# Optimization experiments

Hardware: AMD Instinct MI355X
Metric: run time of the kernel (lower is better)

The kernel has to match this reference:

```python
import jax, jax.numpy as jnp
import numpy as np

# BQQ block dims: Y_sign (p,j,k,m,l), Z_sign (p,j,k,l,n); in=k*n=4096, out=j*m=4096
P, J, K, M, L, N = 2, 32, 32, 128, 16, 128
ACT_BITS = 8  # activation quantization bits


def setup_inputs() -> dict:
    key = jax.random.key(0)
    ks = jax.random.split(key, 7)
    x = jax.random.normal(ks[0], (1, 512, K * N), dtype=jnp.float32)
    # sign matrices in {-1,+1}
    Y_sign = jnp.where(jax.random.normal(ks[1], (P, J, K, M, L)) >= 0, 1.0, -1.0).astype(jnp.float32)
    Z_sign = jnp.where(jax.random.normal(ks[2], (P, J, K, L, N)) >= 0, 1.0, -1.0).astype(jnp.float32)
    # per-block positive scales (abs-mean in the original, so strictly > 0)
    Y_scale = jax.random.uniform(ks[3], (P, J, K, 1, 1), minval=0.01, maxval=0.1, dtype=jnp.float32)
    Z_scale = jax.random.uniform(ks[4], (P, J, K, 1, 1), minval=0.01, maxval=0.1, dtype=jnp.float32)
    A = jax.random.normal(ks[5], (P, J, K, 4), dtype=jnp.float32) * 0.1
    bias = jax.random.normal(ks[6], (J * M,), dtype=jnp.float32) * 0.1
    return {"input": x, "Y_sign": Y_sign, "Z_sign": Z_sign,
            "Y_scale": Y_scale, "Z_scale": Z_scale, "A": A, "bias": bias}


def reference(input, Y_sign, Z_sign, Y_scale, Z_scale, A, bias):
    # --- activation quantization (act_bits = 8, simple round, no STE) ---
    qmax = float(2 ** (ACT_BITS - 1) - 1)  # 127
    x_max = jnp.max(input)
    x_min = jnp.min(input)
    act_scale = jnp.maximum((x_max - x_min) / (2.0 * qmax), 1e-8)
    X = jnp.clip(jnp.round(input / act_scale), -qmax, qmax) * act_scale

    # --- dequantize sign * scale ---
    Y_q = Y_sign * Y_scale  # (p,j,k,m,l)
    Z_q = Z_sign * Z_scale  # (p,j,k,l,n)

    orig_shape = X.shape[:-1]
    X_kn = X.reshape(-1, K, N)  # (B,k,n)

    # chained block einsums
    T = jnp.einsum('bkn,pjkln->bpjkl', X_kn, Z_q)          # (B,p,j,k,l)
    core = jnp.einsum('pjkml,bpjkl->bpjkm', Y_q, T)        # (B,p,j,k,m)

    # quant_bias=True correction terms: A[...,0..3] = (a,b,c,d)
    out1 = jnp.einsum('bpjkm,pjk->bjm', core, A[..., 0])

    Y_sum = Y_q.sum(axis=-1)                               # (p,j,k,m)
    B_coef = jnp.einsum('pjk,pjkm->jkm', A[..., 1], Y_sum)
    Sx = X_kn.sum(axis=-1)                                 # (B,k)
    out2 = jnp.einsum('bk,jkm->bjm', Sx, B_coef)

    Zs = Z_q.sum(axis=-2)                                  # (p,j,k,n)
    Tz = jnp.einsum('bkn,pjkn->bpjk', X_kn, Zs)
    out3 = jnp.einsum('bpjk,pjk->bj', Tz, A[..., 2])

    D_coef = A[..., 3].sum(axis=0)                         # (j,k)
    out4 = jnp.einsum('bk,jk->bj', Sx, D_coef)

    out_bjm = out1 + out2 + (out3 + out4)[:, :, None]      # (B,j,m)
    out_2d = out_bjm.reshape(-1, J * M) + bias
    return out_2d.reshape(*orig_shape, J * M)
```

## Files before the change

### kernel.cpp

```cpp
#include <hip/hip_runtime.h>
#include <hip/hip_bf16.h>

typedef __attribute__((ext_vector_type(4))) float f32x4;
typedef __attribute__((ext_vector_type(8))) short bf16x8;
typedef __attribute__((ext_vector_type(4))) unsigned int u32x4;

#define GLOBAL_AS __attribute__((address_space(1)))
#define LDS_AS __attribute__((address_space(3)))

static __device__ __forceinline__ unsigned short f2bf(float f) {
  __hip_bfloat16 h = __float2bfloat16(f);
  return __builtin_bit_cast(unsigned short, h);
}
static __device__ __forceinline__ float bf2f(unsigned short u) {
  unsigned int v = ((unsigned int)u) << 16;
  return __builtin_bit_cast(float, v);
}
static __device__ __forceinline__ void load_lds16(const void* g, void* l) {
  __builtin_amdgcn_global_load_lds((GLOBAL_AS void*)g, (LDS_AS void*)l, 16, 0, 0);
}

__global__ __launch_bounds__(256) void k_minmax_part(const float* __restrict__ x,
                                                     float* __restrict__ part) {
  int tid = blockIdx.x * 256 + threadIdx.x;
  const float4* xv = (const float4*)x;
  float mn = 3.4e38f, mx = -3.4e38f;
#pragma unroll
  for (int rep = 0; rep < 8; ++rep) {
    float4 v = xv[tid + rep * 65536];
    mn = fminf(mn, fminf(fminf(v.x, v.y), fminf(v.z, v.w)));
    mx = fmaxf(mx, fmaxf(fmaxf(v.x, v.y), fmaxf(v.z, v.w)));
  }
#pragma unroll
  for (int o = 32; o > 0; o >>= 1) {
    mn = fminf(mn, __shfl_down(mn, o));
    mx = fmaxf(mx, __shfl_down(mx, o));
  }
  __shared__ float smn[4], smx[4];
  int lane = threadIdx.x & 63, w = threadIdx.x >> 6;
  if (lane == 0) { smn[w] = mn; smx[w] = mx; }
  __syncthreads();
  if (threadIdx.x == 0) {
    mn = fminf(fminf(smn[0], smn[1]), fminf(smn[2], smn[3]));
    mx = fmaxf(fmaxf(smx[0], smx[1]), fmaxf(smx[2], smx[3]));
    part[2 * blockIdx.x] = mn;
    part[2 * blockIdx.x + 1] = mx;
  }
}

__global__ __launch_bounds__(256) void k_fused(const float* __restrict__ x,
                                               const float* __restrict__ part,
                                               const float* __restrict__ Ysg,
                                               const float* __restrict__ Zsg,
                                               const float* __restrict__ Ysc,
                                               const float* __restrict__ Zsc,
                                               const float* __restrict__ Acoef,
                                               float* __restrict__ scl,
                                               unsigned short* __restrict__ xq,
                                               unsigned short* __restrict__ W) {
  const int t = threadIdx.x;
  if (blockIdx.x < 1024) {
    const int jk = blockIdx.x;
    __shared__ unsigned short Yb[2 * 128 * 24];
    __shared__ unsigned short Zb[128 * 36];
    __shared__ float B1p[2][128];
    __shared__ float C1[128];
    float cf0[2], cf2[2], cf4[2];
    float Dv;
    {
      float ys0 = Ysc[jk], zs0 = Zsc[jk], ys1 = Ysc[1024 + jk], zs1 = Zsc[1024 + jk];
      const float* A0p = Acoef + (size_t)jk * 4;
      const float* A1p = Acoef + (size_t)(1024 + jk) * 4;
      cf0[0] = A0p[0] * ys0 * zs0; cf0[1] = A1p[0] * ys1 * zs1;
      cf2[0] = A0p[1] * ys0;       cf2[1] = A1p[1] * ys1;
      cf4[0] = A0p[2] * zs0;       cf4[1] = A1p[2] * zs1;
      Dv = A0p[3] + A1p[3];
    }
#pragma unroll
    for (int rep = 0; rep < 4; ++rep) {
      int q = rep * 256 + t;
      int l0 = (q & 3) * 4, m = (q >> 2) & 127, p = q >> 9;
      float4 v = *(const float4*)(Ysg + (size_t)(p * 1024 + jk) * 2048 + m * 16 + l0);
      float s4 = v.x + v.y + v.z + v.w;
      s4 += __shfl_xor(s4, 1);
      s4 += __shfl_xor(s4, 2);
      if ((t & 3) == 0) B1p[p][m] = s4;
      float c0 = cf0[p];
      ushort4 o = make_ushort4(f2bf(c0 * v.x), f2bf(c0 * v.y), f2bf(c0 * v.z), f2bf(c0 * v.w));
      *(ushort4*)&Yb[(p * 128 + m) * 24 + l0] = o;
    }
#pragma unroll
    for (int rep = 0; rep < 4; ++rep) {
      int q = rep * 256 + t;
      int n0 = (q & 31) * 4, l = (q >> 5) & 15, p = q >> 9;
      float4 v = *(const float4*)(Zsg + (size_t)(p * 1024 + jk) * 2048 + l * 128 + n0);
      int pl = p * 16 + l;
      Zb[(n0 + 0) * 36 + pl] = f2bf(v.x);
      Zb[(n0 + 1) * 36 + pl] = f2bf(v.y);
      Zb[(n0 + 2) * 36 + pl] = f2bf(v.z);
      Zb[(n0 + 3) * 36 + pl] = f2bf(v.w);
    }
    __syncthreads();
    if (t < 128) {
      float s0 = 0.f, s1 = 0.f;
#pragma unroll
      for (int l = 0; l < 16; ++l) {
        s0 += bf2f(Zb[t * 36 + l]);
        s1 += bf2f(Zb[t * 36 + 16 + l]);
      }
      C1[t] = cf4[0] * s0 + cf4[1] * s1;
    }
    __syncthreads();
    const int lane = t & 63, wid = t >> 6;
    const int wm = wid >> 1, wn = wid & 1;
    const int grp = lane >> 4;
    bf16x8 af[4], bfr[4];
#pragma unroll
    for (int fm = 0; fm < 4; ++fm) {
      int m = wm * 64 + fm * 16 + (lane & 15);
      af[fm] = *(const bf16x8*)((const char*)Yb + ((grp >> 1) * 128 + m) * 48 + (grp & 1) * 16);
    }
#pragma unroll
    for (int fn = 0; fn < 4; ++fn) {
      int n = wn * 64 + fn * 16 + (lane & 15);
      const char* zp = (const char*)Zb + n * 72 + grp * 16;
      uint2 z0 = *(const uint2*)zp;
      uint2 z1 = *(const uint2*)(zp + 8);
      u32x4 zw; zw[0] = z0.x; zw[1] = z0.y; zw[2] = z1.x; zw[3] = z1.y;
      bfr[fn] = __builtin_bit_cast(bf16x8, zw);
    }
    f32x4 acc[4][4];
#pragma unroll
    for (int fm = 0; fm < 4; ++fm)
#pragma unroll
      for (int fn = 0; fn < 4; ++fn)
        acc[fm][fn] = __builtin_amdgcn_mfma_f32_16x16x32_bf16(af[fm], bfr[fn], (f32x4)(0.f), 0, 0, 0);
    const int j = jk >> 5, k = jk & 31;
    float c1v[4];
#pragma unroll
    for (int fn = 0; fn < 4; ++fn) c1v[fn] = C1[wn * 64 + fn * 16 + (lane & 15)];
#pragma unroll
    for (int fm = 0; fm < 4; ++fm) {
#pragma unroll
      for (int i = 0; i < 4; ++i) {
        int row = wm * 64 + fm * 16 + (grp)*4 + i;
        float b1v = cf2[0] * B1p[0][row] + cf2[1] * B1p[1][row] + Dv;
        size_t rowoff = (size_t)(j * 128 + row) * 4096 + (size_t)(k * 128);
#pragma unroll
        for (int fn = 0; fn < 4; ++fn) {
          int col = wn * 64 + fn * 16 + (lane & 15);
          W[rowoff + col] = f2bf(acc[fm][fn][i] + b1v + c1v[fn]);
        }
      }
    }
  } else {
    const int qb = blockIdx.x - 1024;
    float2 v2 = ((const float2*)part)[t];
    float mn = v2.x, mx = v2.y;
#pragma unroll
    for (int o = 32; o > 0; o >>= 1) {
      mn = fminf(mn, __shfl_down(mn, o));
      mx = fmaxf(mx, __shfl_down(mx, o));
    }
    __shared__ float smn2[4], smx2[4], ssc[1];
    int lane = t & 63, w = t >> 6;
    if (lane == 0) { smn2[w] = mn; smx2[w] = mx; }
    __syncthreads();
    if (t == 0) {
      mn = fminf(fminf(smn2[0], smn2[1]), fminf(smn2[2], smn2[3]));
      mx = fmaxf(fmaxf(smx2[0], smx2[1]), fmaxf(smx2[2], smx2[3]));
      ssc[0] = fmaxf((mx - mn) / 254.0f, 1e-8f);
      if (qb == 0) scl[0] = ssc[0];
    }
    __syncthreads();
    const float s = ssc[0];
    int i = qb * 256 + t;
    float4 v = ((const float4*)x)[i];
    float a = fminf(fmaxf(rintf(v.x / s), -127.f), 127.f);
    float b = fminf(fmaxf(rintf(v.y / s), -127.f), 127.f);
    float c = fminf(fmaxf(rintf(v.z / s), -127.f), 127.f);
    float d = fminf(fmaxf(rintf(v.w / s), -127.f), 127.f);
    ((ushort4*)xq)[i] = make_ushort4(f2bf(a), f2bf(b), f2bf(c), f2bf(d));
  }
}

__global__ __launch_bounds__(512) void k_gemm(const unsigned short* __restrict__ Xq,
                                              const unsigned short* __restrict__ W,
                                              unsigned short* __restrict__ P) {
  __shared__ unsigned short Al[2][256 * 64];
  __shared__ unsigned short Bl[2][256 * 64];
  const int t = threadIdx.x, lane = t & 63, wid = t >> 6;
  const int wg = (blockIdx.x & 7) * 32 + (blockIdx.x >> 3);
  const int sk = wg >> 5;
  const int bm = (wg >> 4) & 1;
  const int bn = wg & 15;
  const int wm = wid >> 2, wn = wid & 3;
  const int kbase = sk * 512;
  f32x4 acc[8][4];
#pragma unroll
  for (int a = 0; a < 8; ++a)
#pragma unroll
    for (int b = 0; b < 4; ++b) acc[a][b] = (f32x4)(0.f);

  const int lr = lane >> 3;
  const int lcb = (lane & 7) * 16;

  auto STAGE_A2 = [&](int buf, int kt, int half) {
    const int k0 = kbase + kt * 64;
#pragma unroll
    for (int c = 0; c < 2; ++c) {
      int chunk = wid * 4 + half * 2 + c;
      int r = chunk * 8 + lr;
      int colb = lcb ^ ((r & 7) << 4);
      load_lds16(Xq + ((size_t)(bm * 256 + r) << 12) + k0 + (colb >> 1), &Al[buf][chunk * 512]);
    }
  };
  auto STAGE_B2 = [&](int buf, int kt, int half) {
    const int k0 = kbase + kt * 64;
#pragma unroll
    for (int c = 0; c < 2; ++c) {
      int chunk = wid * 4 + half * 2 + c;
      int r = chunk * 8 + lr;
      int colb = lcb ^ ((r & 7) << 4);
      load_lds16(W + ((size_t)(bn * 256 + r) << 12) + k0 + (colb >> 1), &Bl[buf][chunk * 512]);
    }
  };

  STAGE_A2(0, 0, 0); STAGE_A2(0, 0, 1);
  STAGE_B2(0, 0, 0); STAGE_B2(0, 0, 1);

  for (int it = 0; it < 8; ++it) {
    const int cur = it & 1, nxt = cur ^ 1;
    const int ktn = (it + 1) & 7;
#pragma unroll
    for (int sp = 0; sp < 4; ++sp) {
      if (sp == 0)      STAGE_A2(nxt, ktn, 0);
      else if (sp == 1) STAGE_A2(nxt, ktn, 1);
      else if (sp == 2) STAGE_B2(nxt, ktn, 0);
      else              STAGE_B2(nxt, ktn, 1);
      if (sp == 0) {
        __builtin_amdgcn_sched_barrier(0);
        asm volatile("s_waitcnt vmcnt(2)" ::: "memory");
        __builtin_amdgcn_sched_barrier(0);
        __builtin_amdgcn_s_barrier();
        __builtin_amdgcn_sched_barrier(0);
      }
      const int fmh = sp & 1;
      const int ksh = sp >> 1;
      bf16x8 af[4], bfr[4];
#pragma unroll
      for (int f = 0; f < 4; ++f) {
        int fm = fmh * 4 + f;
        int r = wm * 128 + fm * 16 + (lane & 15);
        int colb = (ksh * 64 + ((lane >> 4) * 16)) ^ ((r & 7) << 4);
        af[f] = *(const bf16x8*)((const char*)&Al[cur][0] + r * 128 + colb);
      }
#pragma unroll
      for (int fn = 0; fn < 4; ++fn) {
        int r = wn * 64 + fn * 16 + (lane & 15);
        int colb = (ksh * 64 + ((lane >> 4) * 16)) ^ ((r & 7) << 4);
        bfr[fn] = *(const bf16x8*)((const char*)&Bl[cur][0] + r * 128 + colb);
      }
      __builtin_amdgcn_sched_barrier(0);
      __builtin_amdgcn_s_setprio(1);
#pragma unroll
      for (int f = 0; f < 4; ++f)
#pragma unroll
        for (int fn = 0; fn < 4; ++fn)
          acc[fmh * 4 + f][fn] =
              __builtin_amdgcn_mfma_f32_16x16x32_bf16(af[f], bfr[fn], acc[fmh * 4 + f][fn], 0, 0, 0);
      __builtin_amdgcn_s_setprio(0);
      __builtin_amdgcn_sched_barrier(0);
    }
    __builtin_amdgcn_s_barrier();
  }

  unsigned short* Pk = P + (size_t)sk * 2097152;
  const int blkL = bm * 16 + bn;
#pragma unroll
  for (int fm = 0; fm < 8; ++fm) {
#pragma unroll
    for (int fn = 0; fn < 4; ++fn) {
      int idx = (((blkL * 8 + wid) * 32 + fm * 4 + fn) * 64) + lane;
      ushort4 o = make_ushort4(f2bf(acc[fm][fn][0]), f2bf(acc[fm][fn][1]),
                               f2bf(acc[fm][fn][2]), f2bf(acc[fm][fn][3]));
      ((ushort4*)Pk)[idx] = o;
    }
  }
}

__global__ __launch_bounds__(256) void k_epi(float* __restrict__ out,
                                             const unsigned short* __restrict__ P,
                                             const float* __restrict__ scl,
                                             const float* __restrict__ bias) {
  int g = blockIdx.x * 256 + threadIdx.x;
  const int lane = g & 63;
  const int ff = (g >> 6) & 31;
  const int fn = ff & 3, fm = ff >> 2;
  const int wid = (g >> 11) & 7;
  const int blkL = g >> 14;
  const int bm = blkL >> 4, bn = blkL & 15;
  const int wm = wid >> 2, wn = wid & 3;
  const int row0 = bm * 256 + wm * 128 + fm * 16 + ((lane >> 4) << 2);
  const int col = bn * 256 + wn * 64 + fn * 16 + (lane & 15);
  const float s = scl[0];
  const float bv = bias[col];
  float sum[4] = {0.f, 0.f, 0.f, 0.f};
#pragma unroll
  for (int k = 0; k < 8; ++k) {
    ushort4 p = ((const ushort4*)(P + (size_t)k * 2097152))[g];
    sum[0] += bf2f(p.x); sum[1] += bf2f(p.y); sum[2] += bf2f(p.z); sum[3] += bf2f(p.w);
  }
#pragma unroll
  for (int i = 0; i < 4; ++i) out[(size_t)(row0 + i) * 4096 + col] = sum[i] * s + bv;
}

__global__ __launch_bounds__(512) void k_gemm_fb(const unsigned short* __restrict__ Xq,
                                                 const unsigned short* __restrict__ W,
                                                 const float* __restrict__ scl,
                                                 const float* __restrict__ bias,
                                                 float* __restrict__ out) {
  __shared__ unsigned short Al[4][128 * 64];
  __shared__ unsigned short Bl[4][64 * 64];
  const int t = threadIdx.x, lane = t & 63, wid = t >> 6;
  const int wg = (blockIdx.x & 7) * 32 + (blockIdx.x >> 3);
  const int bm = wg & 3;
  const int bn = wg >> 2;
  const int wm = wid >> 1, wn = wid & 1;
  f32x4 acc[2][2];
#pragma unroll
  for (int a = 0; a < 2; ++a)
#pragma unroll
    for (int b = 0; b < 2; ++b) acc[a][b] = (f32x4)(0.f);
  const int lr = lane >> 3;
  const int lcb = (lane & 7) * 16;
  auto STAGE = [&](int buf, int kt) {
    const int k0 = kt * 64;
#pragma unroll
    for (int c = 0; c < 2; ++c) {
      int chunk = wid * 2 + c;
      int r = chunk * 8 + lr;
      int colb = lcb ^ ((r & 7) << 4);
      load_lds16(Xq + ((size_t)(bm * 128 + r) << 12) + k0 + (colb >> 1), &Al[buf][chunk * 512]);
    }
    {
      int r = wid * 8 + lr;
      int colb = lcb ^ ((r & 7) << 4);
      load_lds16(W + ((size_t)(bn * 64 + r) << 12) + k0 + (colb >> 1), &Bl[buf][wid * 512]);
    }
  };
  auto COMPUTE = [&](int buf) {
#pragma unroll
    for (int ks = 0; ks < 2; ++ks) {
      bf16x8 af[2], bfr[2];
#pragma unroll
      for (int fm = 0; fm < 2; ++fm) {
        int r = wm * 32 + fm * 16 + (lane & 15);
        int colb = (ks * 64 + ((lane >> 4) * 16)) ^ ((r & 7) << 4);
        af[fm] = *(const bf16x8*)((const char*)&Al[buf][0] + r * 128 + colb);
      }
#pragma unroll
      for (int fn = 0; fn < 2; ++fn) {
        int r = wn * 32 + fn * 16 + (lane & 15);
        int colb = (ks * 64 + ((lane >> 4) * 16)) ^ ((r & 7) << 4);
        bfr[fn] = *(const bf16x8*)((const char*)&Bl[buf][0] + r * 128 + colb);
      }
#pragma unroll
      for (int fm = 0; fm < 2; ++fm)
#pragma unroll
        for (int fn = 0; fn < 2; ++fn)
          acc[fm][fn] = __builtin_amdgcn_mfma_f32_16x16x32_bf16(af[fm], bfr[fn], acc[fm][fn], 0, 0, 0);
    }
  };
  STAGE(0, 0); STAGE(1, 1); STAGE(2, 2);
  for (int t64 = 0; t64 < 64; ++t64) {
    STAGE((t64 + 3) & 3, (t64 + 3) & 63);
    __builtin_amdgcn_sched_barrier(0);
    asm volatile("s_waitcnt vmcnt(9)" ::: "memory");
    __builtin_amdgcn_sched_barrier(0);
    __builtin_amdgcn_s_barrier();
    __builtin_amdgcn_sched_barrier(0);
    COMPUTE(t64 & 3);
    __builtin_amdgcn_sched_barrier(0);
    __builtin_amdgcn_s_barrier();
  }
  const float s = scl[0];
#pragma unroll
  for (int fn = 0; fn < 2; ++fn) {
    int col = bn * 64 + wn * 32 + fn * 16 + (lane & 15);
    float bv = bias[col];
#pragma unroll
    for (int fm = 0; fm < 2; ++fm) {
#pragma unroll
      for (int i = 0; i < 4; ++i) {
        int row = bm * 128 + wm * 32 + fm * 16 + (lane >> 4) * 4 + i;
        out[(size_t)row * 4096 + col] = acc[fm][fn][i] * s + bv;
      }
    }
  }
}

extern "C" void kernel_launch(void* const* d_in, const int* in_sizes, int n_in,
                              void* d_out, int out_size, void* d_ws, size_t ws_size,
                              hipStream_t stream) {
  const float* x    = (const float*)d_in[0];
  const float* Ysg  = (const float*)d_in[1];
  const float* Zsg  = (const float*)d_in[2];
  const float* Ysc  = (const float*)d_in[3];
  const float* Zsc  = (const float*)d_in[4];
  const float* A    = (const float*)d_in[5];
  const float* bias = (const float*)d_in[6];
  float* out = (float*)d_out;

  char* ws = (char*)d_ws;
  float* scl  = (float*)ws;
  float* part = (float*)(ws + 256);
  unsigned short* Xq = (unsigned short*)(ws + 65536);
  unsigned short* W  = (unsigned short*)(ws + 65536 + (size_t)4194304);
  unsigned short* P  = (unsigned short*)(ws + 65536 + (size_t)4194304 + (size_t)33554432);

  k_minmax_part<<<dim3(256), dim3(256), 0, stream>>>(x, part);
  k_fused<<<dim3(3072), dim3(256), 0, stream>>>(x, part, Ysg, Zsg, Ysc, Zsc, A, scl, Xq, W);
  if (ws_size >= (size_t)65536 + 4194304 + 33554432 + 33554432) {
    k_gemm<<<dim3(256), dim3(512), 0, stream>>>(Xq, W, P);
    k_epi<<<dim3(2048), dim3(256), 0, stream>>>(out, P, scl, bias);
  } else {
    k_gemm_fb<<<dim3(256), dim3(512), 0, stream>>>(Xq, W, scl, bias, out);
  }
}
```

Before: 57.97 us.

## Restructure GEMM K-loop to reuse B fragments and interleave LDS reads with MFMA

Replaces the unrolled four-subphase loop with an explicit schedule. B fragments are now read once per K-half and reused across both M-halves, which cuts LDS reads. The next A fragments are issued before the async global-to-LDS staging and an added workgroup barrier, so their latency overlaps with other work. The extra s_barriers and explicit lgkmcnt waits give more control over instruction order, but they add synchronisation that could stall waves.

```diff
diff --git a/kernel.cpp b/kernel.cpp
--- a/kernel.cpp
+++ b/kernel.cpp
@@ -225,6 +225,33 @@
       load_lds16(W + ((size_t)(bn * 256 + r) << 12) + k0 + (colb >> 1), &Bl[buf][chunk * 512]);
     }
   };
+  auto READ_AF = [&](int cur, int fmh, int ksh, bf16x8* af) {
+#pragma unroll
+    for (int f = 0; f < 4; ++f) {
+      int fm = fmh * 4 + f;
+      int r = wm * 128 + fm * 16 + (lane & 15);
+      int colb = (ksh * 64 + ((lane >> 4) * 16)) ^ ((r & 7) << 4);
+      af[f] = *(const bf16x8*)((const char*)&Al[cur][0] + r * 128 + colb);
+    }
+  };
+  auto READ_BF = [&](int cur, int ksh, bf16x8* bfr) {
+#pragma unroll
+    for (int fn = 0; fn < 4; ++fn) {
+      int r = wn * 64 + fn * 16 + (lane & 15);
+      int colb = (ksh * 64 + ((lane >> 4) * 16)) ^ ((r & 7) << 4);
+      bfr[fn] = *(const bf16x8*)((const char*)&Bl[cur][0] + r * 128 + colb);
+    }
+  };
+  auto MFMA16 = [&](int fmh, const bf16x8* af, const bf16x8* bfr) {
+    __builtin_amdgcn_s_setprio(1);
+#pragma unroll
+    for (int f = 0; f < 4; ++f)
+#pragma unroll
+      for (int fn = 0; fn < 4; ++fn)
+        acc[fmh * 4 + f][fn] =
+            __builtin_amdgcn_mfma_f32_16x16x32_bf16(af[f], bfr[fn], acc[fmh * 4 + f][fn], 0, 0, 0);
+    __builtin_amdgcn_s_setprio(0);
+  };
 
   STAGE_A2(0, 0, 0); STAGE_A2(0, 0, 1);
   STAGE_B2(0, 0, 0); STAGE_B2(0, 0, 1);
@@ -232,46 +259,37 @@
   for (int it = 0; it < 8; ++it) {
     const int cur = it & 1, nxt = cur ^ 1;
     const int ktn = (it + 1) & 7;
-#pragma unroll
-    for (int sp = 0; sp < 4; ++sp) {
-      if (sp == 0)      STAGE_A2(nxt, ktn, 0);
-      else if (sp == 1) STAGE_A2(nxt, ktn, 1);
-      else if (sp == 2) STAGE_B2(nxt, ktn, 0);
-      else              STAGE_B2(nxt, ktn, 1);
-      if (sp == 0) {
-        __builtin_amdgcn_sched_barrier(0);
-        asm volatile("s_waitcnt vmcnt(2)" ::: "memory");
-        __builtin_amdgcn_sched_barrier(0);
-        __builtin_amdgcn_s_barrier();
-        __builtin_amdgcn_sched_barrier(0);
-      }
-      const int fmh = sp & 1;
-      const int ksh = sp >> 1;
-      bf16x8 af[4], bfr[4];
-#pragma unroll
-      for (int f = 0; f < 4; ++f) {
-        int fm = fmh * 4 + f;
-        int r = wm * 128 + fm * 16 + (lane & 15);
-        int colb = (ksh * 64 + ((lane >> 4) * 16)) ^ ((r & 7) << 4);
-        af[f] = *(const bf16x8*)((const char*)&Al[cur][0] + r * 128 + colb);
-      }
-#pragma unroll
-      for (int fn = 0; fn < 4; ++fn) {
-        int r = wn * 64 + fn * 16 + (lane & 15);
-        int colb = (ksh * 64 + ((lane >> 4) * 16)) ^ ((r & 7) << 4);
-        bfr[fn] = *(const bf16x8*)((const char*)&Bl[cur][0] + r * 128 + colb);
-      }
-      __builtin_amdgcn_sched_barrier(0);
-      __builtin_amdgcn_s_setprio(1);
-#pragma unroll
-      for (int f = 0; f < 4; ++f)
-#pragma unroll
-        for (int fn = 0; fn < 4; ++fn)
-          acc[fmh * 4 + f][fn] =
-              __builtin_amdgcn_mfma_f32_16x16x32_bf16(af[f], bfr[fn], acc[fmh * 4 + f][fn], 0, 0, 0);
-      __builtin_amdgcn_s_setprio(0);
-      __builtin_amdgcn_sched_barrier(0);
-    }
+    bf16x8 af[4], bfr[4];
+    STAGE_A2(nxt, ktn, 0);
+    __builtin_amdgcn_sched_barrier(0);
+    asm volatile("s_waitcnt vmcnt(2)" ::: "memory");
+    __builtin_amdgcn_sched_barrier(0);
+    __builtin_amdgcn_s_barrier();
+    __builtin_amdgcn_sched_barrier(0);
+    READ_BF(cur, 0, bfr);
+    READ_AF(cur, 0, 0, af);
+    asm volatile("s_waitcnt lgkmcnt(0)" ::: "memory");
+    __builtin_amdgcn_sched_barrier(0);
+    MFMA16(0, af, bfr);
+    READ_AF(cur, 1, 0, af);
+    STAGE_A2(nxt, ktn, 1);
+    __builtin_amdgcn_s_barrier();
+    asm volatile("s_waitcnt lgkmcnt(0)" ::: "memory");
+    __builtin_amdgcn_sched_barrier(0);
+    MFMA16(1, af, bfr);
+    READ_BF(cur, 1, bfr);
+    READ_AF(cur, 0, 1, af);
+    STAGE_B2(nxt, ktn, 0);
+    __builtin_amdgcn_s_barrier();
+    asm volatile("s_waitcnt lgkmcnt(0)" ::: "memory");
+    __builtin_amdgcn_sched_barrier(0);
+    MFMA16(0, af, bfr);
+    READ_AF(cur, 1, 1, af);
+    STAGE_B2(nxt, ktn, 1);
+    __builtin_amdgcn_s_barrier();
+    asm volatile("s_waitcnt lgkmcnt(0)" ::: "memory");
+    __builtin_amdgcn_sched_barrier(0);
+    MFMA16(1, af, bfr);
     __builtin_amdgcn_s_barrier();
   }
 
```

Measured after the change: 56.41 us. 2.7% less time.
